# Kernel tuning notes

Hardware: AMD Instinct MI355X
Metric: run time of the kernel (lower is better)

The kernel has to match this reference:

```python
import jax, jax.numpy as jnp
import numpy as np

N_NODES = 100000
N_EDGES = 600000
N_GRAPHS = 8
D_IN = 256
H = 128
N_CONV = 2  # layers [128,128,128] -> first_h + 2 GINConvs
BN_EPS = 1e-5


def _bn_eval(x, p):
    # p: [4, H] rows = (gamma, beta, running_mean, running_var); eval-mode BatchNorm1d
    g, b, m, v = p[0], p[1], p[2], p[3]
    return (x - m) * jax.lax.rsqrt(v + BN_EPS) * g + b


def setup_inputs() -> dict:
    key = jax.random.key(0)
    ks = jax.random.split(key, 12)
    x = jax.random.normal(ks[0], (N_NODES, D_IN), dtype=jnp.float32)
    edge_index = jax.random.randint(ks[1], (2, N_EDGES), 0, N_NODES, dtype=jnp.int64 if jax.config.jax_enable_x64 else jnp.int32)
    batch = jnp.sort(jax.random.randint(ks[2], (N_NODES,), 0, N_GRAPHS))
    s = 0.05
    w_first = jax.random.normal(ks[3], (D_IN, H), dtype=jnp.float32) * s
    b_first = jax.random.normal(ks[4], (H,), dtype=jnp.float32) * s

    def bn_params(k):
        k1, k2, k3, k4 = jax.random.split(k, 4)
        gamma = jax.random.uniform(k1, (H,), minval=0.5, maxval=1.5)
        beta = jax.random.normal(k2, (H,)) * 0.1
        mean = jax.random.normal(k3, (H,)) * 0.1
        var = jax.random.uniform(k4, (H,), minval=0.5, maxval=1.5)
        return jnp.stack([gamma, beta, mean, var])  # [4, H]

    bn_first = bn_params(ks[5])
    w_conv = jax.random.normal(ks[6], (N_CONV, H, H), dtype=jnp.float32) * s
    b_conv = jax.random.normal(ks[7], (N_CONV, H), dtype=jnp.float32) * s
    bn_conv = jnp.stack([bn_params(k) for k in jax.random.split(ks[8], N_CONV)])  # [2,4,H]
    w_lin = jax.random.normal(ks[9], (N_CONV + 1, H, 1), dtype=jnp.float32) * s
    b_lin = jax.random.normal(ks[10], (N_CONV + 1, 1), dtype=jnp.float32) * s
    return {"x": x, "edge_index": edge_index, "batch": batch,
            "w_first": w_first, "b_first": b_first, "bn_first": bn_first,
            "w_conv": w_conv, "b_conv": b_conv, "bn_conv": bn_conv,
            "w_lin": w_lin, "b_lin": b_lin}


def reference(x, edge_index, batch, w_first, b_first, bn_first, w_conv, b_conv, bn_conv, w_lin, b_lin):
    src, dst = edge_index[0], edge_index[1]
    # first_h: Linear + BN(eval) + ReLU
    h = jax.nn.relu(_bn_eval(x @ w_first + b_first, bn_first))  # [N, H]

    # layer 0: node-level linear head + global max pool
    node_pred = h @ w_lin[0] + b_lin[0]  # [N, 1]
    wsi_pred = jax.ops.segment_max(node_pred, batch, num_segments=N_GRAPHS)  # [G, 1]

    for l in range(N_CONV):
        # GINConv (eps=0, sum aggregation): nn((1+eps)*x_i + sum_{j->i} x_j)
        agg = jax.ops.segment_sum(h[src], dst, num_segments=N_NODES)  # [N, H]
        h = jax.nn.relu(_bn_eval((h + agg) @ w_conv[l] + b_conv[l], bn_conv[l]))
        np_sub = h @ w_lin[l + 1] + b_lin[l + 1]  # [N, 1]
        node_pred = node_pred + np_sub
        wsi_pred = wsi_pred + jax.ops.segment_max(np_sub, batch, num_segments=N_GRAPHS)
        # dropout p=0.0 -> identity
    return wsi_pred, node_pred
```

## Files before the change

### kernel.cpp

```cpp
#include <hip/hip_runtime.h>
#include <hip/hip_bf16.h>

#define H 128
#define D_IN 256
#define NGRAPH 8

typedef __attribute__((ext_vector_type(8))) short bf16x8;
typedef __attribute__((ext_vector_type(4))) float f32x4;
typedef __attribute__((ext_vector_type(4))) int i32x4;

__device__ __forceinline__ unsigned fenc(float f) {
  unsigned u = __float_as_uint(f);
  return (u & 0x80000000u) ? ~u : (u | 0x80000000u);
}
__device__ __forceinline__ float fdec(unsigned e) {
  unsigned v = (e & 0x80000000u) ? (e & 0x7FFFFFFFu) : ~e;
  return __uint_as_float(v);
}
__device__ __forceinline__ unsigned short f2bf(float f) {
  unsigned u = __float_as_uint(f);
  unsigned r = u + 0x7FFFu + ((u >> 16) & 1u);
  return (unsigned short)(r >> 16);
}

__device__ __forceinline__ void gload16(const void* gsrc, void* ldst) {
  __builtin_amdgcn_global_load_lds(
      (const __attribute__((address_space(1))) unsigned int*)gsrc,
      (__attribute__((address_space(3))) unsigned int*)ldst, 16, 0, 0);
}

__global__ void init_kernel(int* __restrict__ offsets, int n1) {
  int i = blockIdx.x * blockDim.x + threadIdx.x;
  if (i < n1) offsets[i] = 0;
}

__global__ void count_kernel(const int* __restrict__ dst, int* __restrict__ offsets, int E) {
  int i = blockIdx.x * blockDim.x + threadIdx.x;
  int stride = gridDim.x * blockDim.x;
  for (int e = i; e < E; e += stride) atomicAdd(&offsets[dst[e]], 1);
}

__global__ void __launch_bounds__(1024)
scan_local(int* __restrict__ data, int* __restrict__ bsum, int n) {
  __shared__ int s[1024];
  int tid = threadIdx.x;
  int i = blockIdx.x * 1024 + tid;
  int v = (i < n) ? data[i] : 0;
  s[tid] = v;
  __syncthreads();
  for (int off = 1; off < 1024; off <<= 1) {
    int t = (tid >= off) ? s[tid - off] : 0;
    __syncthreads();
    s[tid] += t;
    __syncthreads();
  }
  if (i < n) data[i] = s[tid] - v;
  if (tid == 1023) bsum[blockIdx.x] = s[1023];
}

__global__ void __launch_bounds__(128)
scan_bsum(int* __restrict__ bsum, int nb) {
  __shared__ int s[128];
  int tid = threadIdx.x;
  int v = (tid < nb) ? bsum[tid] : 0;
  s[tid] = v;
  __syncthreads();
  for (int off = 1; off < 128; off <<= 1) {
    int t = (tid >= off) ? s[tid - off] : 0;
    __syncthreads();
    s[tid] += t;
    __syncthreads();
  }
  if (tid < nb) bsum[tid] = s[tid] - v;
}

__global__ void __launch_bounds__(1024)
scan_add(int* __restrict__ data, const int* __restrict__ bsum, int* __restrict__ cursor,
         int n, int ncur) {
  int i = blockIdx.x * 1024 + threadIdx.x;
  if (i < n) {
    int v = data[i] + bsum[blockIdx.x];
    data[i] = v;
    if (i < ncur) cursor[i] = v;
  }
}

__global__ void fill_kernel(const int* __restrict__ src, const int* __restrict__ dst,
                            int* __restrict__ cursor, int* __restrict__ esrc, int E) {
  int i = blockIdx.x * blockDim.x + threadIdx.x;
  int stride = gridDim.x * blockDim.x;
  for (int e = i; e < E; e += stride) {
    int d = dst[e];
    int p = atomicAdd(&cursor[d], 1);
    esrc[p] = src[e];
  }
}

__global__ void prep_weights(const float* __restrict__ wf, const float* __restrict__ wcv,
                             unsigned short* __restrict__ Bf, unsigned short* __restrict__ Bc) {
  int i = blockIdx.x * 256 + threadIdx.x;
  if (i < 32768) {
    int s = i >> 12, r = i & 4095;
    int c = r >> 5, r2 = r & 31;
    int g = r2 >> 3, j = r2 & 7;
    int k = s * 32 + g * 8 + j;
    Bf[i] = f2bf(wf[k * H + c]);
  } else {
    int i2 = i - 32768;
    int l = i2 >> 14, r = i2 & 16383;
    int s = r >> 12, rr = r & 4095;
    int c = rr >> 5, r2 = rr & 31;
    int g = r2 >> 3, j = r2 & 7;
    int k = s * 32 + g * 8 + j;
    Bc[i2] = f2bf(wcv[l * H * H + k * H + c]);
  }
}

template <int K, bool AF32, bool FIRST>
__global__ void __launch_bounds__(256, 4)
gemm_kernel(const void* __restrict__ Ain, const unsigned short* __restrict__ Bpack,
            const float* __restrict__ bias, const float* __restrict__ bn,
            const float* __restrict__ wlin, const float* __restrict__ blin, int lidx,
            const int* __restrict__ batch, unsigned short* __restrict__ hout,
            float* __restrict__ node_pred, unsigned* __restrict__ slot, int N) {
  constexpr int RB = 256;
  constexpr int ROWBYTES = AF32 ? K * 4 : K * 2;
  constexpr int NCHUNK = ROWBYTES / RB;
  constexpr int SPC = AF32 ? 2 : 4;
  __shared__ char s_a[64 * RB];
  __shared__ float s_head[64][2];
  __shared__ unsigned s_wsi[NGRAPH];
  const int tid = threadIdx.x;
  const int wid = tid >> 6, lane = tid & 63;
  const int wr = wid >> 1, wc = wid & 1;
  const int g = lane >> 4, l15 = lane & 15;
  const int row0blk = blockIdx.x * 64;
  if (tid < NGRAPH) s_wsi[tid] = 0u;

  f32x4 acc[2][4] = {};
  const int lrow0 = wr * 32;
  const char* Ab = (const char*)Ain;

  for (int ch = 0; ch < NCHUNK; ++ch) {
#pragma unroll
    for (int it = 0; it < 4; ++it) {
      int unit = it * 256 + tid;
      int lr = unit >> 4;
      int cb = (unit & 15) * 16;
      int grow = row0blk + lr;
      grow = (grow < N) ? grow : (N - 1);
      int gcol = cb ^ ((lr & 7) << 4);
      gload16(Ab + (size_t)grow * ROWBYTES + ch * RB + gcol,
              s_a + (it * 256 + wid * 64) * 16);
    }
    __syncthreads();

#pragma unroll
    for (int s = 0; s < SPC; ++s) {
      int sg = ch * SPC + s;
      bf16x8 bfr[4];
#pragma unroll
      for (int n = 0; n < 4; ++n) {
        int c = wc * 64 + n * 16 + l15;
        bfr[n] = *(const bf16x8*)(Bpack + sg * 4096 + c * 32 + g * 8);
      }
      bf16x8 af[2];
#pragma unroll
      for (int m = 0; m < 2; ++m) {
        int lr = lrow0 + m * 16 + l15;
        int sw = (lr & 7) << 4;
        if (AF32) {
          int c0 = s * 128 + g * 32;
          f32x4 u0 = *(const f32x4*)(s_a + lr * RB + (c0 ^ sw));
          f32x4 u1 = *(const f32x4*)(s_a + lr * RB + ((c0 + 16) ^ sw));
          union { unsigned short hh[8]; bf16x8 v; } pk;
          pk.hh[0] = f2bf(u0[0]); pk.hh[1] = f2bf(u0[1]);
          pk.hh[2] = f2bf(u0[2]); pk.hh[3] = f2bf(u0[3]);
          pk.hh[4] = f2bf(u1[0]); pk.hh[5] = f2bf(u1[1]);
          pk.hh[6] = f2bf(u1[2]); pk.hh[7] = f2bf(u1[3]);
          af[m] = pk.v;
        } else {
          int c0 = s * 64 + g * 16;
          af[m] = *(const bf16x8*)(s_a + lr * RB + (c0 ^ sw));
        }
      }
#pragma unroll
      for (int m = 0; m < 2; ++m)
#pragma unroll
        for (int n = 0; n < 4; ++n)
          acc[m][n] = __builtin_amdgcn_mfma_f32_16x16x32_bf16(af[m], bfr[n], acc[m][n], 0, 0, 0);
    }
    __syncthreads();
  }

  float sc[4], sh[4], wl[4];
#pragma unroll
  for (int n = 0; n < 4; ++n) {
    int c = wc * 64 + n * 16 + l15;
    float gam = bn[c], bet = bn[H + c], mu = bn[2 * H + c], va = bn[3 * H + c];
    float rs = rsqrtf(va + 1e-5f);
    sc[n] = gam * rs;
    sh[n] = (bias[c] - mu) * gam * rs + bet;
    wl[n] = wlin[c];
  }

  char* aw = s_a + wid * 2048;
#pragma unroll
  for (int m = 0; m < 2; ++m) {
    float pj[4] = {0.f, 0.f, 0.f, 0.f};
#pragma unroll
    for (int n = 0; n < 4; ++n)
#pragma unroll
      for (int j = 0; j < 4; ++j) {
        float hv = fmaxf(acc[m][n][j] * sc[n] + sh[n], 0.f);
        pj[j] += hv * wl[n];
        *(unsigned short*)(aw + (g * 4 + j) * 128 + (n * 16 + l15) * 2) = f2bf(hv);
      }
#pragma unroll
    for (int j = 0; j < 4; ++j) {
      pj[j] += __shfl_xor(pj[j], 1);
      pj[j] += __shfl_xor(pj[j], 2);
      pj[j] += __shfl_xor(pj[j], 4);
      pj[j] += __shfl_xor(pj[j], 8);
    }
    if (l15 == 0) {
#pragma unroll
      for (int j = 0; j < 4; ++j)
        s_head[wr * 32 + m * 16 + g * 4 + j][wc] = pj[j];
    }
    int grb = row0blk + wr * 32 + m * 16;
#pragma unroll
    for (int it = 0; it < 2; ++it) {
      int bo = lane * 16 + it * 1024;
      int r16 = bo >> 7, inrow = bo & 127;
      if (grb + r16 < N)
        *(i32x4*)((char*)hout + (size_t)(grb + r16) * 256 + wc * 128 + inrow) =
            *(i32x4*)(aw + bo);
    }
  }
  __syncthreads();
  if (tid < 64) {
    int grh = row0blk + tid;
    if (grh < N) {
      float np = s_head[tid][0] + s_head[tid][1] + blin[lidx];
      if (FIRST) node_pred[grh] = np; else node_pred[grh] += np;
      atomicMax(&s_wsi[batch[grh]], fenc(np));
    }
  }
  __syncthreads();
  if (tid < NGRAPH) slot[blockIdx.x * NGRAPH + tid] = s_wsi[tid];
}

__global__ void __launch_bounds__(256)
agg_kernel(const unsigned short* __restrict__ h, const int* __restrict__ offsets,
           const int* __restrict__ esrc, unsigned short* __restrict__ tmp, int n) {
  int node = blockIdx.x * 4 + (threadIdx.x >> 6);
  if (node >= n) return;
  int lane = threadIdx.x & 63;
  const unsigned* hw = (const unsigned*)h;
  size_t base = (size_t)node * (H / 2) + lane;
  unsigned u = hw[base];
  float a0 = __uint_as_float((u & 0xFFFFu) << 16);
  float a1 = __uint_as_float(u & 0xFFFF0000u);
  int s = offsets[node], e = offsets[node + 1];
  int j = s;
  for (; j + 4 <= e; j += 4) {
    int i0 = esrc[j], i1 = esrc[j + 1], i2 = esrc[j + 2], i3 = esrc[j + 3];
    unsigned v0 = hw[(size_t)i0 * (H / 2) + lane];
    unsigned v1 = hw[(size_t)i1 * (H / 2) + lane];
    unsigned v2 = hw[(size_t)i2 * (H / 2) + lane];
    unsigned v3 = hw[(size_t)i3 * (H / 2) + lane];
    a0 += __uint_as_float((v0 & 0xFFFFu) << 16) + __uint_as_float((v1 & 0xFFFFu) << 16) +
          __uint_as_float((v2 & 0xFFFFu) << 16) + __uint_as_float((v3 & 0xFFFFu) << 16);
    a1 += __uint_as_float(v0 & 0xFFFF0000u) + __uint_as_float(v1 & 0xFFFF0000u) +
          __uint_as_float(v2 & 0xFFFF0000u) + __uint_as_float(v3 & 0xFFFF0000u);
  }
  for (; j < e; ++j) {
    unsigned v2 = hw[(size_t)esrc[j] * (H / 2) + lane];
    a0 += __uint_as_float((v2 & 0xFFFFu) << 16);
    a1 += __uint_as_float(v2 & 0xFFFF0000u);
  }
  unsigned r = ((unsigned)f2bf(a1) << 16) | (unsigned)f2bf(a0);
  ((unsigned*)tmp)[base] = r;
}

__global__ void __launch_bounds__(256)
finalize_kernel(const unsigned* __restrict__ slots, float* __restrict__ out, int nb) {
  __shared__ float red[3][NGRAPH];
  int tid = threadIdx.x;
  if (tid < 192) {
    int pair = tid >> 3, w = tid & 7;
    int l = pair >> 3, g = pair & 7;
    unsigned m = 0u;
    const unsigned* base = slots + (size_t)l * nb * NGRAPH + g;
    for (int b = w; b < nb; b += 8) m = max(m, base[b * NGRAPH]);
    m = max(m, (unsigned)__shfl_xor((int)m, 1));
    m = max(m, (unsigned)__shfl_xor((int)m, 2));
    m = max(m, (unsigned)__shfl_xor((int)m, 4));
    if (w == 0) red[l][g] = fdec(m);
  }
  __syncthreads();
  if (tid < NGRAPH) out[tid] = red[0][tid] + red[1][tid] + red[2][tid];
}

extern "C" void kernel_launch(void* const* d_in, const int* in_sizes, int n_in,
                              void* d_out, int out_size, void* d_ws, size_t ws_size,
                              hipStream_t stream) {
  const float* x        = (const float*)d_in[0];
  const int*   ei       = (const int*)d_in[1];
  const int*   batch    = (const int*)d_in[2];
  const float* w_first  = (const float*)d_in[3];
  const float* b_first  = (const float*)d_in[4];
  const float* bn_first = (const float*)d_in[5];
  const float* w_conv   = (const float*)d_in[6];
  const float* b_conv   = (const float*)d_in[7];
  const float* bn_conv  = (const float*)d_in[8];
  const float* w_lin    = (const float*)d_in[9];
  const float* b_lin    = (const float*)d_in[10];
  float* out = (float*)d_out;

  const int N = in_sizes[0] / D_IN;
  const int E = in_sizes[1] / 2;
  const int* src = ei;
  const int* dst = ei + E;

  const int gemm_grid = (N + 63) / 64;

  char* ws = (char*)d_ws;
  unsigned short* h   = (unsigned short*)ws;
  unsigned short* tmp = h + (size_t)N * H;
  unsigned short* wTf = tmp + (size_t)N * H;
  unsigned short* wTc = wTf + H * D_IN;
  int* offsets = (int*)(wTc + 2 * H * H);
  int* cursor  = offsets + (N + 1);
  int* esrc    = cursor + N;
  int* bsum    = esrc + E;
  unsigned* slots = (unsigned*)(bsum + 128);
  float* node_pred = out + NGRAPH;

  const int nscan = N + 1;
  const int nb = (nscan + 1023) / 1024;

  init_kernel<<<(N + 256) / 256, 256, 0, stream>>>(offsets, N + 1);
  count_kernel<<<1024, 256, 0, stream>>>(dst, offsets, E);
  scan_local<<<nb, 1024, 0, stream>>>(offsets, bsum, nscan);
  scan_bsum<<<1, 128, 0, stream>>>(bsum, nb);
  scan_add<<<nb, 1024, 0, stream>>>(offsets, bsum, cursor, nscan, N);
  fill_kernel<<<1024, 256, 0, stream>>>(src, dst, cursor, esrc, E);
  prep_weights<<<256, 256, 0, stream>>>(w_first, w_conv, wTf, wTc);

  gemm_kernel<D_IN, true, true><<<gemm_grid, 256, 0, stream>>>(
      x, wTf, b_first, bn_first, w_lin, b_lin, 0, batch, h, node_pred, slots, N);
  for (int l = 0; l < 2; ++l) {
    agg_kernel<<<(N + 3) / 4, 256, 0, stream>>>(h, offsets, esrc, tmp, N);
    gemm_kernel<H, false, false><<<gemm_grid, 256, 0, stream>>>(
        tmp, wTc + (size_t)l * 16384, b_conv + (size_t)l * H, bn_conv + (size_t)l * 4 * H,
        w_lin + (size_t)(l + 1) * H, b_lin, l + 1, batch, h, node_pred,
        slots + (size_t)(l + 1) * gemm_grid * NGRAPH, N);
  }
  finalize_kernel<<<1, 256, 0, stream>>>(slots, out, gemm_grid);
}
```

Measured before the change: 253.1 us.

## Merge setup kernels and double GEMM row tile to 128 with 512 threads

Folds weight packing into the offsets-init kernel and merges the block-sum scan into the scan-add kernel, with every block redoing the small 128-entry scan, so two launches disappear. The GEMM now processes 128 rows per block with 512 threads (8 waves) instead of 64 rows with 256 threads, which halves the grid and the per-block epilogue overhead. The cost is twice the LDS per block and different occupancy. The per-block slot count also halves, and finalize still reads gemm_grid entries, so it stays consistent.

```diff
diff --git a/kernel.cpp b/kernel.cpp
--- a/kernel.cpp
+++ b/kernel.cpp
@@ -29,9 +29,26 @@
       (__attribute__((address_space(3))) unsigned int*)ldst, 16, 0, 0);
 }
 
-__global__ void init_kernel(int* __restrict__ offsets, int n1) {
-  int i = blockIdx.x * blockDim.x + threadIdx.x;
+__global__ void init_prep_kernel(int* __restrict__ offsets, int n1,
+                                 const float* __restrict__ wf, const float* __restrict__ wcv,
+                                 unsigned short* __restrict__ Bf, unsigned short* __restrict__ Bc) {
+  int i = blockIdx.x * 256 + threadIdx.x;
   if (i < n1) offsets[i] = 0;
+  if (i < 32768) {
+    int s = i >> 12, r = i & 4095;
+    int c = r >> 5, r2 = r & 31;
+    int g = r2 >> 3, j = r2 & 7;
+    int k = s * 32 + g * 8 + j;
+    Bf[i] = f2bf(wf[k * H + c]);
+  } else if (i < 65536) {
+    int i2 = i - 32768;
+    int l = i2 >> 14, r = i2 & 16383;
+    int s = r >> 12, rr = r & 4095;
+    int c = rr >> 5, r2 = rr & 31;
+    int g = r2 >> 3, j = r2 & 7;
+    int k = s * 32 + g * 8 + j;
+    Bc[i2] = f2bf(wcv[l * H * H + k * H + c]);
+  }
 }
 
 __global__ void count_kernel(const int* __restrict__ dst, int* __restrict__ offsets, int E) {
@@ -58,28 +75,23 @@
   if (tid == 1023) bsum[blockIdx.x] = s[1023];
 }
 
-__global__ void __launch_bounds__(128)
-scan_bsum(int* __restrict__ bsum, int nb) {
-  __shared__ int s[128];
+__global__ void __launch_bounds__(1024)
+scan_add2(int* __restrict__ data, const int* __restrict__ bsum, int* __restrict__ cursor,
+          int n, int ncur, int nb) {
+  __shared__ int sb[128];
   int tid = threadIdx.x;
-  int v = (tid < nb) ? bsum[tid] : 0;
-  s[tid] = v;
+  if (tid < 128) sb[tid] = (tid < nb) ? bsum[tid] : 0;
   __syncthreads();
   for (int off = 1; off < 128; off <<= 1) {
-    int t = (tid >= off) ? s[tid - off] : 0;
-    __syncthreads();
-    s[tid] += t;
-    __syncthreads();
-  }
-  if (tid < nb) bsum[tid] = s[tid] - v;
-}
-
-__global__ void __launch_bounds__(1024)
-scan_add(int* __restrict__ data, const int* __restrict__ bsum, int* __restrict__ cursor,
-         int n, int ncur) {
-  int i = blockIdx.x * 1024 + threadIdx.x;
+    int t = (tid < 128 && tid >= off) ? sb[tid - off] : 0;
+    __syncthreads();
+    if (tid < 128) sb[tid] += t;
+    __syncthreads();
+  }
+  int add = (blockIdx.x == 0) ? 0 : sb[blockIdx.x - 1];
+  int i = blockIdx.x * 1024 + tid;
   if (i < n) {
-    int v = data[i] + bsum[blockIdx.x];
+    int v = data[i] + add;
     data[i] = v;
     if (i < ncur) cursor[i] = v;
   }
@@ -96,28 +108,8 @@
   }
 }
 
-__global__ void prep_weights(const float* __restrict__ wf, const float* __restrict__ wcv,
-                             unsigned short* __restrict__ Bf, unsigned short* __restrict__ Bc) {
-  int i = blockIdx.x * 256 + threadIdx.x;
-  if (i < 32768) {
-    int s = i >> 12, r = i & 4095;
-    int c = r >> 5, r2 = r & 31;
-    int g = r2 >> 3, j = r2 & 7;
-    int k = s * 32 + g * 8 + j;
-    Bf[i] = f2bf(wf[k * H + c]);
-  } else {
-    int i2 = i - 32768;
-    int l = i2 >> 14, r = i2 & 16383;
-    int s = r >> 12, rr = r & 4095;
-    int c = rr >> 5, r2 = rr & 31;
-    int g = r2 >> 3, j = r2 & 7;
-    int k = s * 32 + g * 8 + j;
-    Bc[i2] = f2bf(wcv[l * H * H + k * H + c]);
-  }
-}
-
 template <int K, bool AF32, bool FIRST>
-__global__ void __launch_bounds__(256, 4)
+__global__ void __launch_bounds__(512, 2)
 gemm_kernel(const void* __restrict__ Ain, const unsigned short* __restrict__ Bpack,
             const float* __restrict__ bias, const float* __restrict__ bn,
             const float* __restrict__ wlin, const float* __restrict__ blin, int lidx,
@@ -127,31 +119,31 @@
   constexpr int ROWBYTES = AF32 ? K * 4 : K * 2;
   constexpr int NCHUNK = ROWBYTES / RB;
   constexpr int SPC = AF32 ? 2 : 4;
-  __shared__ char s_a[64 * RB];
-  __shared__ float s_head[64][2];
+  __shared__ char s_a[128 * RB];
+  __shared__ float s_head[128][2];
   __shared__ unsigned s_wsi[NGRAPH];
   const int tid = threadIdx.x;
   const int wid = tid >> 6, lane = tid & 63;
-  const int wr = wid >> 1, wc = wid & 1;
+  const int wrow = wid >> 1, wcol = wid & 1;
   const int g = lane >> 4, l15 = lane & 15;
-  const int row0blk = blockIdx.x * 64;
+  const int row0blk = blockIdx.x * 128;
   if (tid < NGRAPH) s_wsi[tid] = 0u;
 
   f32x4 acc[2][4] = {};
-  const int lrow0 = wr * 32;
+  const int lrow0 = wrow * 32;
   const char* Ab = (const char*)Ain;
 
   for (int ch = 0; ch < NCHUNK; ++ch) {
 #pragma unroll
     for (int it = 0; it < 4; ++it) {
-      int unit = it * 256 + tid;
+      int unit = it * 512 + tid;
       int lr = unit >> 4;
       int cb = (unit & 15) * 16;
       int grow = row0blk + lr;
       grow = (grow < N) ? grow : (N - 1);
       int gcol = cb ^ ((lr & 7) << 4);
       gload16(Ab + (size_t)grow * ROWBYTES + ch * RB + gcol,
-              s_a + (it * 256 + wid * 64) * 16);
+              s_a + (it * 512 + wid * 64) * 16);
     }
     __syncthreads();
 
@@ -161,7 +153,7 @@
       bf16x8 bfr[4];
 #pragma unroll
       for (int n = 0; n < 4; ++n) {
-        int c = wc * 64 + n * 16 + l15;
+        int c = wcol * 64 + n * 16 + l15;
         bfr[n] = *(const bf16x8*)(Bpack + sg * 4096 + c * 32 + g * 8);
       }
       bf16x8 af[2];
@@ -196,7 +188,7 @@
   float sc[4], sh[4], wl[4];
 #pragma unroll
   for (int n = 0; n < 4; ++n) {
-    int c = wc * 64 + n * 16 + l15;
+    int c = wcol * 64 + n * 16 + l15;
     float gam = bn[c], bet = bn[H + c], mu = bn[2 * H + c], va = bn[3 * H + c];
     float rs = rsqrtf(va + 1e-5f);
     sc[n] = gam * rs;
@@ -226,20 +218,20 @@
     if (l15 == 0) {
 #pragma unroll
       for (int j = 0; j < 4; ++j)
-        s_head[wr * 32 + m * 16 + g * 4 + j][wc] = pj[j];
-    }
-    int grb = row0blk + wr * 32 + m * 16;
+        s_head[wrow * 32 + m * 16 + g * 4 + j][wcol] = pj[j];
+    }
+    int grb = row0blk + wrow * 32 + m * 16;
 #pragma unroll
     for (int it = 0; it < 2; ++it) {
       int bo = lane * 16 + it * 1024;
       int r16 = bo >> 7, inrow = bo & 127;
       if (grb + r16 < N)
-        *(i32x4*)((char*)hout + (size_t)(grb + r16) * 256 + wc * 128 + inrow) =
+        *(i32x4*)((char*)hout + (size_t)(grb + r16) * 256 + wcol * 128 + inrow) =
             *(i32x4*)(aw + bo);
     }
   }
   __syncthreads();
-  if (tid < 64) {
+  if (tid < 128) {
     int grh = row0blk + tid;
     if (grh < N) {
       float np = s_head[tid][0] + s_head[tid][1] + blin[lidx];
@@ -324,7 +316,7 @@
   const int* src = ei;
   const int* dst = ei + E;
 
-  const int gemm_grid = (N + 63) / 64;
+  const int gemm_grid = (N + 127) / 128;
 
   char* ws = (char*)d_ws;
   unsigned short* h   = (unsigned short*)ws;
@@ -341,19 +333,18 @@
   const int nscan = N + 1;
   const int nb = (nscan + 1023) / 1024;
 
-  init_kernel<<<(N + 256) / 256, 256, 0, stream>>>(offsets, N + 1);
+  init_prep_kernel<<<(N + 256) / 256, 256, 0, stream>>>(offsets, N + 1, w_first, w_conv,
+                                                        wTf, wTc);
   count_kernel<<<1024, 256, 0, stream>>>(dst, offsets, E);
   scan_local<<<nb, 1024, 0, stream>>>(offsets, bsum, nscan);
-  scan_bsum<<<1, 128, 0, stream>>>(bsum, nb);
-  scan_add<<<nb, 1024, 0, stream>>>(offsets, bsum, cursor, nscan, N);
+  scan_add2<<<nb, 1024, 0, stream>>>(offsets, bsum, cursor, nscan, N, nb);
   fill_kernel<<<1024, 256, 0, stream>>>(src, dst, cursor, esrc, E);
-  prep_weights<<<256, 256, 0, stream>>>(w_first, w_conv, wTf, wTc);
-
-  gemm_kernel<D_IN, true, true><<<gemm_grid, 256, 0, stream>>>(
+
+  gemm_kernel<D_IN, true, true><<<gemm_grid, 512, 0, stream>>>(
       x, wTf, b_first, bn_first, w_lin, b_lin, 0, batch, h, node_pred, slots, N);
   for (int l = 0; l < 2; ++l) {
     agg_kernel<<<(N + 3) / 4, 256, 0, stream>>>(h, offsets, esrc, tmp, N);
-    gemm_kernel<H, false, false><<<gemm_grid, 256, 0, stream>>>(
+    gemm_kernel<H, false, false><<<gemm_grid, 512, 0, stream>>>(
         tmp, wTc + (size_t)l * 16384, b_conv + (size_t)l * H, bn_conv + (size_t)l * 4 * H,
         w_lin + (size_t)(l + 1) * H, b_lin, l + 1, batch, h, node_pred,
         slots + (size_t)(l + 1) * gemm_grid * NGRAPH, N);
```

Measured after the change: 257.7 us. About the same (+1.8%).
